# Kernel optimization log

Measured on AMD Instinct MI355X. Metric: run time of the kernel, lower is better.

## Reference

```python
import jax, jax.numpy as jnp
import numpy as np

B, N, DIM, H, DH = 2, 2048, 256, 4, 32


def setup_inputs() -> dict:
    key = jax.random.key(0)
    k0, k1, k2, k3, k4 = jax.random.split(key, 5)
    x = jax.random.normal(k0, (B, N, DIM), dtype=jnp.float32)
    pos_bias = jax.random.normal(k1, (H, N, N), dtype=jnp.float32) * 0.02
    focus_present_mask = jax.random.randint(k2, (B,), 0, 2).astype(bool)
    W_qkv = jax.random.normal(k3, (DIM, 3 * H * DH), dtype=jnp.float32) * 0.05
    W_out = jax.random.normal(k4, (H * DH, DIM), dtype=jnp.float32) * 0.05
    return {"x": x, "pos_bias": pos_bias, "focus_present_mask": focus_present_mask,
            "W_qkv": W_qkv, "W_out": W_out}


def reference(x, pos_bias, focus_present_mask, W_qkv, W_out):
    b, n, _ = x.shape
    scale = DH ** -0.5
    qkv = x @ W_qkv                                  # [b, n, 3*h*dh]
    q, k, v = jnp.split(qkv, 3, axis=-1)
    split_heads = lambda t: t.reshape(b, n, H, DH).transpose(0, 2, 1, 3)  # b h n d
    q, k, v = split_heads(q), split_heads(k), split_heads(v)
    q = q * scale
    sim = jnp.einsum('bhid,bhjd->bhij', q, k)        # [b, h, n, n]
    sim = sim + pos_bias[None]                       # additive relative-position bias
    # focus-present masking: batches with mask=True attend only to self (eye),
    # batches with mask=False attend everywhere -> always-apply form is equivalent.
    eye = jnp.eye(n, dtype=bool)
    mask = jnp.where(focus_present_mask[:, None, None, None], eye[None, None], True)
    neg = -jnp.finfo(sim.dtype).max
    sim = jnp.where(mask, sim, neg)
    sim = sim - jax.lax.stop_gradient(sim.max(axis=-1, keepdims=True))
    attn = jax.nn.softmax(sim, axis=-1)
    out = jnp.einsum('bhij,bhjd->bhid', attn, v)     # [b, h, n, d]
    out = out.transpose(0, 2, 1, 3).reshape(b, n, H * DH)
    return out @ W_out
```

## Files before the change

### kernel.cpp

```cpp
#include <hip/hip_runtime.h>
#include <hip/hip_bf16.h>

#define DEVI __device__ __forceinline__

typedef short bf16x8 __attribute__((ext_vector_type(8)));
typedef float f32x4 __attribute__((ext_vector_type(4)));
typedef unsigned short u16x4 __attribute__((ext_vector_type(4)));

static constexpr int B_ = 2, N_ = 2048, DIM_ = 256, H_ = 4, DH_ = 32;
static constexpr int NQKV_ = 3 * H_ * DH_;
static constexpr float SCALE_ = 0.17677669529663687f;

DEVI unsigned short f2bf(float f) {
  __hip_bfloat16 h = __float2bfloat16(f);
  return *reinterpret_cast<unsigned short*>(&h);
}

__global__ __launch_bounds__(256) void k_gemm_qkv(
    const float* __restrict__ X,
    const float* __restrict__ Wqkv,
    unsigned short* __restrict__ Qo,
    unsigned short* __restrict__ Ko,
    unsigned short* __restrict__ Vo,
    unsigned short* __restrict__ Vto) {
  constexpr int LDB = 258;
  __shared__ unsigned short Bts[64 * LDB];
  const int tid = threadIdx.x;
  const int col0b = blockIdx.y * 64;
  for (int p = tid; p < 64 * 256; p += 256) {
    const int col = p & 63;
    const int k = p >> 6;
    Bts[col * LDB + k] = f2bf(Wqkv[k * NQKV_ + col0b + col]);
  }
  __syncthreads();

  const int w = tid >> 6, l = tid & 63;
  const int lr = l & 15, g = l >> 4;
  const int row0 = blockIdx.x * 64 + (w >> 1) * 32;
  const int colw = (w & 1) * 32;
  const float* xr0 = X + (size_t)(row0 + lr) * 256;
  const float* xr1 = X + (size_t)(row0 + 16 + lr) * 256;
  f32x4 acc[2][2] = {};
#pragma unroll
  for (int kb = 0; kb < 256; kb += 32) {
    f32x4 xa = *(const f32x4*)(xr0 + kb + g * 8);
    f32x4 xb4 = *(const f32x4*)(xr0 + kb + g * 8 + 4);
    f32x4 xc = *(const f32x4*)(xr1 + kb + g * 8);
    f32x4 xd = *(const f32x4*)(xr1 + kb + g * 8 + 4);
    bf16x8 a0, a1;
#pragma unroll
    for (int j = 0; j < 4; j++) {
      a0[j] = (short)f2bf(xa[j]);
      a0[4 + j] = (short)f2bf(xb4[j]);
      a1[j] = (short)f2bf(xc[j]);
      a1[4 + j] = (short)f2bf(xd[j]);
    }
    bf16x8 b0 = *(const bf16x8*)(&Bts[(colw + lr) * LDB + kb + g * 8]);
    bf16x8 b1 = *(const bf16x8*)(&Bts[(colw + 16 + lr) * LDB + kb + g * 8]);
    acc[0][0] = __builtin_amdgcn_mfma_f32_16x16x32_bf16(a0, b0, acc[0][0], 0, 0, 0);
    acc[0][1] = __builtin_amdgcn_mfma_f32_16x16x32_bf16(a0, b1, acc[0][1], 0, 0, 0);
    acc[1][0] = __builtin_amdgcn_mfma_f32_16x16x32_bf16(a1, b0, acc[1][0], 0, 0, 0);
    acc[1][1] = __builtin_amdgcn_mfma_f32_16x16x32_bf16(a1, b1, acc[1][1], 0, 0, 0);
  }
#pragma unroll
  for (int mi = 0; mi < 2; mi++)
#pragma unroll
    for (int ni = 0; ni < 2; ni++) {
      const int colg = col0b + colw + ni * 16 + lr;
      const int sec = colg >> 7;
      const int h = (colg >> 5) & 3;
      const int d = colg & 31;
      const int rbase = row0 + mi * 16 + g * 4;
      const int bb = rbase >> 11;
      const int n0 = rbase & (N_ - 1);
      if (sec == 0) {
#pragma unroll
        for (int r = 0; r < 4; r++)
          Qo[((bb * H_ + h) * N_ + n0 + r) * DH_ + d] = f2bf(acc[mi][ni][r] * SCALE_);
      } else if (sec == 1) {
#pragma unroll
        for (int r = 0; r < 4; r++)
          Ko[((bb * H_ + h) * N_ + n0 + r) * DH_ + d] = f2bf(acc[mi][ni][r]);
      } else {
        u16x4 vp;
#pragma unroll
        for (int r = 0; r < 4; r++) {
          const unsigned short vb = f2bf(acc[mi][ni][r]);
          Vo[((bb * H_ + h) * N_ + n0 + r) * DH_ + d] = vb;
          vp[r] = vb;
        }
        const int c32 = n0 & ~31;
        const int local = n0 & 31;
        const int slot = ((local & 15) >> 2) * 8 + ((local >> 4) << 2);
        *(u16x4*)(Vto + ((bb * H_ + h) * DH_ + d) * N_ + c32 + slot) = vp;
      }
    }
}

__global__ __launch_bounds__(512) void k_attn_lds(
    const unsigned short* __restrict__ Q,
    const unsigned short* __restrict__ K,
    const unsigned short* __restrict__ Vt,
    const unsigned short* __restrict__ V,
    const float* __restrict__ bias,
    const int* __restrict__ mask,
    unsigned short* __restrict__ AO) {
  const int bh = blockIdx.y;
  const int b = bh >> 2, h = bh & 3;
  const int qt = blockIdx.x;
  const int tid = threadIdx.x;
  const int qb = qt * 16;
  if (mask[b] != 0) {
    if (tid < 64) {
      const int q = tid >> 2;
      const int d8 = (tid & 3) * 8;
      bf16x8 v = *(const bf16x8*)(V + ((size_t)bh * N_ + qb + q) * DH_ + d8);
      *(bf16x8*)(AO + (size_t)(b * N_ + qb + q) * (H_ * DH_) + h * DH_ + d8) = v;
    }
    return;
  }
  __shared__ float so[16][8][32];
  __shared__ float ss[16][8];
  const int w = tid >> 6, l = tid & 63, lr = l & 15, g = l >> 4;
  const int c0 = w * 256;
  const unsigned short* Kp = K + bh * N_ * DH_;
  const unsigned short* Vtp = Vt + bh * DH_ * N_;
  const float* biasrow = bias + (size_t)(h * N_ + qb + lr) * N_;
  const bf16x8 qf = *(const bf16x8*)(Q + (bh * N_ + qb + lr) * DH_ + g * 8);
  float s = 0.f;
  f32x4 o0 = {}, o1 = {};
  for (int c = c0; c < c0 + 256; c += 32) {
    bf16x8 k0 = *(const bf16x8*)(Kp + (c + lr) * DH_ + g * 8);
    bf16x8 k1 = *(const bf16x8*)(Kp + (c + 16 + lr) * DH_ + g * 8);
    f32x4 z = {};
    f32x4 st0 = __builtin_amdgcn_mfma_f32_16x16x32_bf16(k0, qf, z, 0, 0, 0);
    f32x4 st1 = __builtin_amdgcn_mfma_f32_16x16x32_bf16(k1, qf, z, 0, 0, 0);
    f32x4 bi0 = *(const f32x4*)(biasrow + c + g * 4);
    f32x4 bi1 = *(const f32x4*)(biasrow + c + 16 + g * 4);
    bf16x8 pf;
#pragma unroll
    for (int r = 0; r < 4; r++) {
      const float p0 = __expf(st0[r] + bi0[r]);
      const float p1 = __expf(st1[r] + bi1[r]);
      s += p0 + p1;
      pf[r] = (short)f2bf(p0);
      pf[4 + r] = (short)f2bf(p1);
    }
    bf16x8 v0 = *(const bf16x8*)(Vtp + lr * N_ + c + g * 8);
    bf16x8 v1 = *(const bf16x8*)(Vtp + (16 + lr) * N_ + c + g * 8);
    o0 = __builtin_amdgcn_mfma_f32_16x16x32_bf16(v0, pf, o0, 0, 0, 0);
    o1 = __builtin_amdgcn_mfma_f32_16x16x32_bf16(v1, pf, o1, 0, 0, 0);
  }
  s += __shfl_xor(s, 16);
  s += __shfl_xor(s, 32);
  *(f32x4*)&so[lr][w][g * 4] = o0;
  *(f32x4*)&so[lr][w][16 + g * 4] = o1;
  if (g == 0) ss[lr][w] = s;
  __syncthreads();
  {
    const int q = tid >> 5;
    const int d = tid & 31;
    float acc = 0.f, ssum = 0.f;
#pragma unroll
    for (int w2 = 0; w2 < 8; w2++) {
      acc += so[q][w2][d];
      ssum += ss[q][w2];
    }
    AO[(size_t)(b * N_ + qb + q) * (H_ * DH_) + h * DH_ + d] = f2bf(acc / ssum);
  }
}

__global__ __launch_bounds__(256) void k_gemm_out(
    const unsigned short* __restrict__ A,
    const float* __restrict__ Wout,
    float* __restrict__ out) {
  constexpr int LDB = 130;
  __shared__ unsigned short Bts[64 * LDB];
  const int tid = threadIdx.x;
  const int col0b = blockIdx.y * 64;
  for (int p = tid; p < 64 * 128; p += 256) {
    const int col = p & 63;
    const int k = p >> 6;
    Bts[col * LDB + k] = f2bf(Wout[k * 256 + col0b + col]);
  }
  __syncthreads();

  const int w = tid >> 6, l = tid & 63;
  const int lr = l & 15, g = l >> 4;
  const int row0 = blockIdx.x * 64 + (w >> 1) * 32;
  const int colw = (w & 1) * 32;
  f32x4 acc[2][2] = {};
#pragma unroll
  for (int kb = 0; kb < 128; kb += 32) {
    bf16x8 a0 = *(const bf16x8*)(A + (row0 + lr) * 128 + kb + g * 8);
    bf16x8 a1 = *(const bf16x8*)(A + (row0 + 16 + lr) * 128 + kb + g * 8);
    bf16x8 b0 = *(const bf16x8*)(&Bts[(colw + lr) * LDB + kb + g * 8]);
    bf16x8 b1 = *(const bf16x8*)(&Bts[(colw + 16 + lr) * LDB + kb + g * 8]);
    acc[0][0] = __builtin_amdgcn_mfma_f32_16x16x32_bf16(a0, b0, acc[0][0], 0, 0, 0);
    acc[0][1] = __builtin_amdgcn_mfma_f32_16x16x32_bf16(a0, b1, acc[0][1], 0, 0, 0);
    acc[1][0] = __builtin_amdgcn_mfma_f32_16x16x32_bf16(a1, b0, acc[1][0], 0, 0, 0);
    acc[1][1] = __builtin_amdgcn_mfma_f32_16x16x32_bf16(a1, b1, acc[1][1], 0, 0, 0);
  }
#pragma unroll
  for (int mi = 0; mi < 2; mi++)
#pragma unroll
    for (int ni = 0; ni < 2; ni++) {
      const int colg = col0b + colw + ni * 16 + lr;
      const int rbase = row0 + mi * 16 + g * 4;
#pragma unroll
      for (int r = 0; r < 4; r++)
        out[(size_t)(rbase + r) * 256 + colg] = acc[mi][ni][r];
    }
}

extern "C" void kernel_launch(void* const* d_in, const int* in_sizes, int n_in,
                              void* d_out, int out_size, void* d_ws, size_t ws_size,
                              hipStream_t stream) {
  const float* x = (const float*)d_in[0];
  const float* bias = (const float*)d_in[1];
  const int* mask = (const int*)d_in[2];
  const float* Wqkv = (const float*)d_in[3];
  const float* Wout = (const float*)d_in[4];
  float* out = (float*)d_out;
  char* ws = (char*)d_ws;

  unsigned short* Qb    = (unsigned short*)(ws + 0);
  unsigned short* Kb    = (unsigned short*)(ws + 1048576);
  unsigned short* Vb    = (unsigned short*)(ws + 2097152);
  unsigned short* Vtb   = (unsigned short*)(ws + 3145728);
  unsigned short* AOb   = (unsigned short*)(ws + 4194304);

  k_gemm_qkv<<<dim3(64, 6), dim3(256), 0, stream>>>(x, Wqkv, Qb, Kb, Vb, Vtb);
  k_attn_lds<<<dim3(128, B_ * H_), dim3(512), 0, stream>>>(
      Qb, Kb, Vtb, Vb, bias, mask, AOb);
  k_gemm_out<<<dim3(64, 4), dim3(256), 0, stream>>>(AOb, Wout, out);
}
```

Baseline: 45.04 us.

## Stage pos_bias tiles through double-buffered LDS with coalesced row loads

```diff
diff --git a/kernel.cpp b/kernel.cpp
--- a/kernel.cpp
+++ b/kernel.cpp
@@ -119,37 +119,64 @@
     }
     return;
   }
+  constexpr int LDBS = 258;
   __shared__ float so[16][8][32];
   __shared__ float ss[16][8];
+  __shared__ float bs[2][16][LDBS];
   const int w = tid >> 6, l = tid & 63, lr = l & 15, g = l >> 4;
-  const int c0 = w * 256;
+  const int srow = tid >> 5;
+  const int sidx = tid & 31;
+  const float* brow_g = bias + (size_t)(h * N_ + qb + srow) * N_;
   const unsigned short* Kp = K + bh * N_ * DH_;
   const unsigned short* Vtp = Vt + bh * DH_ * N_;
-  const float* biasrow = bias + (size_t)(h * N_ + qb + lr) * N_;
   const bf16x8 qf = *(const bf16x8*)(Q + (bh * N_ + qb + lr) * DH_ + g * 8);
+  {
+    f32x4 p0 = *(const f32x4*)(brow_g + sidx * 4);
+    f32x4 p1 = *(const f32x4*)(brow_g + 128 + sidx * 4);
+    *(f32x4*)&bs[0][srow][sidx * 4] = p0;
+    *(f32x4*)&bs[0][srow][128 + sidx * 4] = p1;
+  }
+  __syncthreads();
   float s = 0.f;
   f32x4 o0 = {}, o1 = {};
-  for (int c = c0; c < c0 + 256; c += 32) {
-    bf16x8 k0 = *(const bf16x8*)(Kp + (c + lr) * DH_ + g * 8);
-    bf16x8 k1 = *(const bf16x8*)(Kp + (c + 16 + lr) * DH_ + g * 8);
-    f32x4 z = {};
-    f32x4 st0 = __builtin_amdgcn_mfma_f32_16x16x32_bf16(k0, qf, z, 0, 0, 0);
-    f32x4 st1 = __builtin_amdgcn_mfma_f32_16x16x32_bf16(k1, qf, z, 0, 0, 0);
-    f32x4 bi0 = *(const f32x4*)(biasrow + c + g * 4);
-    f32x4 bi1 = *(const f32x4*)(biasrow + c + 16 + g * 4);
-    bf16x8 pf;
-#pragma unroll
-    for (int r = 0; r < 4; r++) {
-      const float p0 = __expf(st0[r] + bi0[r]);
-      const float p1 = __expf(st1[r] + bi1[r]);
-      s += p0 + p1;
-      pf[r] = (short)f2bf(p0);
-      pf[4 + r] = (short)f2bf(p1);
-    }
-    bf16x8 v0 = *(const bf16x8*)(Vtp + lr * N_ + c + g * 8);
-    bf16x8 v1 = *(const bf16x8*)(Vtp + (16 + lr) * N_ + c + g * 8);
-    o0 = __builtin_amdgcn_mfma_f32_16x16x32_bf16(v0, pf, o0, 0, 0, 0);
-    o1 = __builtin_amdgcn_mfma_f32_16x16x32_bf16(v1, pf, o1, 0, 0, 0);
+  int cur = 0;
+#pragma unroll
+  for (int ci = 0; ci < 8; ci++) {
+    f32x4 n0 = {}, n1 = {};
+    if (ci < 7) {
+      n0 = *(const f32x4*)(brow_g + (ci + 1) * 256 + sidx * 4);
+      n1 = *(const f32x4*)(brow_g + (ci + 1) * 256 + 128 + sidx * 4);
+    }
+    {
+      const int c = ci * 256 + w * 32;
+      bf16x8 k0 = *(const bf16x8*)(Kp + (c + lr) * DH_ + g * 8);
+      bf16x8 k1 = *(const bf16x8*)(Kp + (c + 16 + lr) * DH_ + g * 8);
+      f32x4 z = {};
+      f32x4 st0 = __builtin_amdgcn_mfma_f32_16x16x32_bf16(k0, qf, z, 0, 0, 0);
+      f32x4 st1 = __builtin_amdgcn_mfma_f32_16x16x32_bf16(k1, qf, z, 0, 0, 0);
+      f32x4 bi0 = *(const f32x4*)(&bs[cur][lr][w * 32 + g * 4]);
+      f32x4 bi1 = *(const f32x4*)(&bs[cur][lr][w * 32 + 16 + g * 4]);
+      bf16x8 pf;
+#pragma unroll
+      for (int r = 0; r < 4; r++) {
+        const float p0 = __expf(st0[r] + bi0[r]);
+        const float p1 = __expf(st1[r] + bi1[r]);
+        s += p0 + p1;
+        pf[r] = (short)f2bf(p0);
+        pf[4 + r] = (short)f2bf(p1);
+      }
+      bf16x8 v0 = *(const bf16x8*)(Vtp + lr * N_ + c + g * 8);
+      bf16x8 v1 = *(const bf16x8*)(Vtp + (16 + lr) * N_ + c + g * 8);
+      o0 = __builtin_amdgcn_mfma_f32_16x16x32_bf16(v0, pf, o0, 0, 0, 0);
+      o1 = __builtin_amdgcn_mfma_f32_16x16x32_bf16(v1, pf, o1, 0, 0, 0);
+    }
+    __syncthreads();
+    if (ci < 7) {
+      *(f32x4*)&bs[cur ^ 1][srow][sidx * 4] = n0;
+      *(f32x4*)&bs[cur ^ 1][srow][128 + sidx * 4] = n1;
+    }
+    __syncthreads();
+    cur ^= 1;
   }
   s += __shfl_xor(s, 16);
   s += __shfl_xor(s, 32);
```

After: 41.61 us. -7.6%, faster.

## Split attention keys across two blocks and merge partials in output GEMM

Applied to the files above, without the earlier changes.

```diff
diff --git a/kernel.cpp b/kernel.cpp
--- a/kernel.cpp
+++ b/kernel.cpp
@@ -14,6 +14,11 @@
 DEVI unsigned short f2bf(float f) {
   __hip_bfloat16 h = __float2bfloat16(f);
   return *reinterpret_cast<unsigned short*>(&h);
+}
+DEVI float bf2f(unsigned short u) {
+  union { unsigned int i; float f; } x;
+  x.i = ((unsigned int)u) << 16;
+  return x.f;
 }
 
 __global__ __launch_bounds__(256) void k_gemm_qkv(
@@ -97,60 +102,91 @@
     }
 }
 
-__global__ __launch_bounds__(512) void k_attn_lds(
+__global__ __launch_bounds__(512, 6) void k_attn_split2(
     const unsigned short* __restrict__ Q,
     const unsigned short* __restrict__ K,
     const unsigned short* __restrict__ Vt,
-    const unsigned short* __restrict__ V,
     const float* __restrict__ bias,
     const int* __restrict__ mask,
-    unsigned short* __restrict__ AO) {
-  const int bh = blockIdx.y;
+    float* __restrict__ PO,
+    float* __restrict__ PS) {
+  const int bh = blockIdx.z;
   const int b = bh >> 2, h = bh & 3;
-  const int qt = blockIdx.x;
+  if (mask[b] != 0) return;
+  const int qt = blockIdx.x, sp = blockIdx.y;
   const int tid = threadIdx.x;
   const int qb = qt * 16;
-  if (mask[b] != 0) {
-    if (tid < 64) {
-      const int q = tid >> 2;
-      const int d8 = (tid & 3) * 8;
-      bf16x8 v = *(const bf16x8*)(V + ((size_t)bh * N_ + qb + q) * DH_ + d8);
-      *(bf16x8*)(AO + (size_t)(b * N_ + qb + q) * (H_ * DH_) + h * DH_ + d8) = v;
-    }
-    return;
-  }
+  const int spbase = sp * 1024;
   __shared__ float so[16][8][32];
   __shared__ float ss[16][8];
+  __shared__ unsigned short bs[3][16][258];
   const int w = tid >> 6, l = tid & 63, lr = l & 15, g = l >> 4;
-  const int c0 = w * 256;
+  const int srow = tid >> 5;
+  const int sidx = tid & 31;
+  const float* brow = bias + (size_t)(h * N_ + qb + srow) * N_ + spbase;
   const unsigned short* Kp = K + bh * N_ * DH_;
   const unsigned short* Vtp = Vt + bh * DH_ * N_;
-  const float* biasrow = bias + (size_t)(h * N_ + qb + lr) * N_;
   const bf16x8 qf = *(const bf16x8*)(Q + (bh * N_ + qb + lr) * DH_ + g * 8);
   float s = 0.f;
   f32x4 o0 = {}, o1 = {};
-  for (int c = c0; c < c0 + 256; c += 32) {
-    bf16x8 k0 = *(const bf16x8*)(Kp + (c + lr) * DH_ + g * 8);
-    bf16x8 k1 = *(const bf16x8*)(Kp + (c + 16 + lr) * DH_ + g * 8);
-    f32x4 z = {};
-    f32x4 st0 = __builtin_amdgcn_mfma_f32_16x16x32_bf16(k0, qf, z, 0, 0, 0);
-    f32x4 st1 = __builtin_amdgcn_mfma_f32_16x16x32_bf16(k1, qf, z, 0, 0, 0);
-    f32x4 bi0 = *(const f32x4*)(biasrow + c + g * 4);
-    f32x4 bi1 = *(const f32x4*)(biasrow + c + 16 + g * 4);
-    bf16x8 pf;
-#pragma unroll
-    for (int r = 0; r < 4; r++) {
-      const float p0 = __expf(st0[r] + bi0[r]);
-      const float p1 = __expf(st1[r] + bi1[r]);
-      s += p0 + p1;
-      pf[r] = (short)f2bf(p0);
-      pf[4 + r] = (short)f2bf(p1);
-    }
-    bf16x8 v0 = *(const bf16x8*)(Vtp + lr * N_ + c + g * 8);
-    bf16x8 v1 = *(const bf16x8*)(Vtp + (16 + lr) * N_ + c + g * 8);
-    o0 = __builtin_amdgcn_mfma_f32_16x16x32_bf16(v0, pf, o0, 0, 0, 0);
-    o1 = __builtin_amdgcn_mfma_f32_16x16x32_bf16(v1, pf, o1, 0, 0, 0);
-  }
+
+#define BLOAD(PA, PB, CI)                                        \
+  {                                                              \
+    PA = *(const f32x4*)(brow + (CI) * 256 + sidx * 4);          \
+    PB = *(const f32x4*)(brow + (CI) * 256 + 128 + sidx * 4);    \
+  }
+#define BSTORE(BUF, PA, PB)                                      \
+  {                                                              \
+    u16x4 ua, ub;                                                \
+    _Pragma("unroll") for (int r = 0; r < 4; r++) {              \
+      ua[r] = f2bf(PA[r]);                                       \
+      ub[r] = f2bf(PB[r]);                                       \
+    }                                                            \
+    *(u16x4*)&bs[BUF][srow][sidx * 4] = ua;                      \
+    *(u16x4*)&bs[BUF][srow][128 + sidx * 4] = ub;                \
+  }
+#define ABODY(CI)                                                             \
+  {                                                                           \
+    const int c = spbase + (CI) * 256 + w * 32;                               \
+    bf16x8 k0 = *(const bf16x8*)(Kp + (c + lr) * DH_ + g * 8);                \
+    bf16x8 k1 = *(const bf16x8*)(Kp + (c + 16 + lr) * DH_ + g * 8);           \
+    f32x4 z = {};                                                             \
+    f32x4 st0 = __builtin_amdgcn_mfma_f32_16x16x32_bf16(k0, qf, z, 0, 0, 0);  \
+    f32x4 st1 = __builtin_amdgcn_mfma_f32_16x16x32_bf16(k1, qf, z, 0, 0, 0);  \
+    u16x4 ua = *(const u16x4*)&bs[(CI) % 3][lr][w * 32 + g * 4];              \
+    u16x4 ub = *(const u16x4*)&bs[(CI) % 3][lr][w * 32 + 16 + g * 4];         \
+    bf16x8 pf;                                                                \
+    _Pragma("unroll") for (int r = 0; r < 4; r++) {                           \
+      const float p0 = __expf(st0[r] + bf2f(ua[r]));                          \
+      const float p1 = __expf(st1[r] + bf2f(ub[r]));                          \
+      s += p0 + p1;                                                           \
+      pf[r] = (short)f2bf(p0);                                                \
+      pf[4 + r] = (short)f2bf(p1);                                            \
+    }                                                                         \
+    bf16x8 v0 = *(const bf16x8*)(Vtp + lr * N_ + c + g * 8);                  \
+    bf16x8 v1 = *(const bf16x8*)(Vtp + (16 + lr) * N_ + c + g * 8);           \
+    o0 = __builtin_amdgcn_mfma_f32_16x16x32_bf16(v0, pf, o0, 0, 0, 0);        \
+    o1 = __builtin_amdgcn_mfma_f32_16x16x32_bf16(v1, pf, o1, 0, 0, 0);        \
+  }
+
+  f32x4 pA0, pA1, pB0, pB1;
+  BLOAD(pA0, pA1, 0)
+  BLOAD(pB0, pB1, 1)
+  BSTORE(0, pA0, pA1)
+  __syncthreads();
+  BSTORE(1, pB0, pB1)
+  BLOAD(pA0, pA1, 2)
+  ABODY(0)
+  __syncthreads();
+  BSTORE(2, pA0, pA1)
+  BLOAD(pB0, pB1, 3)
+  ABODY(1)
+  __syncthreads();
+  BSTORE(0, pB0, pB1)
+  ABODY(2)
+  __syncthreads();
+  ABODY(3)
+
   s += __shfl_xor(s, 16);
   s += __shfl_xor(s, 32);
   *(f32x4*)&so[lr][w][g * 4] = o0;
@@ -166,12 +202,17 @@
       acc += so[q][w2][d];
       ssum += ss[q][w2];
     }
-    AO[(size_t)(b * N_ + qb + q) * (H_ * DH_) + h * DH_ + d] = f2bf(acc / ssum);
-  }
+    PO[((size_t)(bh * 2 + sp) * N_ + qb + q) * 32 + d] = acc;
+    if (d == 0) PS[(size_t)(bh * 2 + sp) * N_ + qb + q] = ssum;
+  }
+#undef BLOAD
+#undef BSTORE
+#undef ABODY
 }
 
 __global__ __launch_bounds__(256) void k_gemm_out(
-    const unsigned short* __restrict__ A,
+    const float* __restrict__ PO, const float* __restrict__ PS,
+    const unsigned short* __restrict__ V, const int* __restrict__ mask,
     const float* __restrict__ Wout,
     float* __restrict__ out) {
   constexpr int LDB = 130;
@@ -189,11 +230,41 @@
   const int lr = l & 15, g = l >> 4;
   const int row0 = blockIdx.x * 64 + (w >> 1) * 32;
   const int colw = (w & 1) * 32;
+  const int b = (blockIdx.x * 64) >> 11;
+  const bool msk = (mask[b] != 0);
+  const int na = (row0 + lr) & (N_ - 1);
+  const int nb2 = (row0 + 16 + lr) & (N_ - 1);
   f32x4 acc[2][2] = {};
 #pragma unroll
   for (int kb = 0; kb < 128; kb += 32) {
-    bf16x8 a0 = *(const bf16x8*)(A + (row0 + lr) * 128 + kb + g * 8);
-    bf16x8 a1 = *(const bf16x8*)(A + (row0 + 16 + lr) * 128 + kb + g * 8);
+    const int h = kb >> 5;
+    const int d0 = g * 8;
+    const int bh = b * H_ + h;
+    bf16x8 a0, a1;
+    if (msk) {
+      a0 = *(const bf16x8*)(V + ((size_t)bh * N_ + na) * DH_ + d0);
+      a1 = *(const bf16x8*)(V + ((size_t)bh * N_ + nb2) * DH_ + d0);
+    } else {
+      const size_t base0 = (size_t)(bh * 2 + 0) * N_;
+      const size_t base1 = (size_t)(bh * 2 + 1) * N_;
+      f32x4 xa0 = *(const f32x4*)(PO + (base0 + na) * 32 + d0);
+      f32x4 xa0h = *(const f32x4*)(PO + (base0 + na) * 32 + d0 + 4);
+      f32x4 xa1 = *(const f32x4*)(PO + (base1 + na) * 32 + d0);
+      f32x4 xa1h = *(const f32x4*)(PO + (base1 + na) * 32 + d0 + 4);
+      const float ia = 1.f / (PS[base0 + na] + PS[base1 + na]);
+      f32x4 xb0 = *(const f32x4*)(PO + (base0 + nb2) * 32 + d0);
+      f32x4 xb0h = *(const f32x4*)(PO + (base0 + nb2) * 32 + d0 + 4);
+      f32x4 xb1 = *(const f32x4*)(PO + (base1 + nb2) * 32 + d0);
+      f32x4 xb1h = *(const f32x4*)(PO + (base1 + nb2) * 32 + d0 + 4);
+      const float ib = 1.f / (PS[base0 + nb2] + PS[base1 + nb2]);
+#pragma unroll
+      for (int j = 0; j < 4; j++) {
+        a0[j] = (short)f2bf((xa0[j] + xa1[j]) * ia);
+        a0[4 + j] = (short)f2bf((xa0h[j] + xa1h[j]) * ia);
+        a1[j] = (short)f2bf((xb0[j] + xb1[j]) * ib);
+        a1[4 + j] = (short)f2bf((xb0h[j] + xb1h[j]) * ib);
+      }
+    }
     bf16x8 b0 = *(const bf16x8*)(&Bts[(colw + lr) * LDB + kb + g * 8]);
     bf16x8 b1 = *(const bf16x8*)(&Bts[(colw + 16 + lr) * LDB + kb + g * 8]);
     acc[0][0] = __builtin_amdgcn_mfma_f32_16x16x32_bf16(a0, b0, acc[0][0], 0, 0, 0);
@@ -224,14 +295,15 @@
   float* out = (float*)d_out;
   char* ws = (char*)d_ws;
 
-  unsigned short* Qb    = (unsigned short*)(ws + 0);
-  unsigned short* Kb    = (unsigned short*)(ws + 1048576);
-  unsigned short* Vb    = (unsigned short*)(ws + 2097152);
-  unsigned short* Vtb   = (unsigned short*)(ws + 3145728);
-  unsigned short* AOb   = (unsigned short*)(ws + 4194304);
+  unsigned short* Qb  = (unsigned short*)(ws + 0);
+  unsigned short* Kb  = (unsigned short*)(ws + 1048576);
+  unsigned short* Vb  = (unsigned short*)(ws + 2097152);
+  unsigned short* Vtb = (unsigned short*)(ws + 3145728);
+  float* PO           = (float*)(ws + 4194304);
+  float* PS           = (float*)(ws + 8388608);
 
   k_gemm_qkv<<<dim3(64, 6), dim3(256), 0, stream>>>(x, Wqkv, Qb, Kb, Vb, Vtb);
-  k_attn_lds<<<dim3(128, B_ * H_), dim3(512), 0, stream>>>(
-      Qb, Kb, Vtb, Vb, bias, mask, AOb);
-  k_gemm_out<<<dim3(64, 4), dim3(256), 0, stream>>>(AOb, Wout, out);
-}
+  k_attn_split2<<<dim3(128, 2, B_ * H_), dim3(512), 0, stream>>>(
+      Qb, Kb, Vtb, bias, mask, PO, PS);
+  k_gemm_out<<<dim3(64, 4), dim3(256), 0, stream>>>(PO, PS, Vb, mask, Wout, out);
+}
```

After: 49.65 us. +10.2%, slower.

## Split attention key range across two blocks and add combine kernel

Applied to the files above, without the earlier changes.

```diff
diff --git a/kernel.cpp b/kernel.cpp
--- a/kernel.cpp
+++ b/kernel.cpp
@@ -97,39 +97,33 @@
     }
 }
 
-__global__ __launch_bounds__(512) void k_attn_lds(
+__global__ __launch_bounds__(512, 6) void k_attn2(
     const unsigned short* __restrict__ Q,
     const unsigned short* __restrict__ K,
     const unsigned short* __restrict__ Vt,
-    const unsigned short* __restrict__ V,
     const float* __restrict__ bias,
     const int* __restrict__ mask,
-    unsigned short* __restrict__ AO) {
-  const int bh = blockIdx.y;
+    float* __restrict__ PO,
+    float* __restrict__ PS) {
+  const int bh = blockIdx.z;
   const int b = bh >> 2, h = bh & 3;
-  const int qt = blockIdx.x;
+  if (mask[b] != 0) return;
+  const int qt = blockIdx.x, sp = blockIdx.y;
   const int tid = threadIdx.x;
   const int qb = qt * 16;
-  if (mask[b] != 0) {
-    if (tid < 64) {
-      const int q = tid >> 2;
-      const int d8 = (tid & 3) * 8;
-      bf16x8 v = *(const bf16x8*)(V + ((size_t)bh * N_ + qb + q) * DH_ + d8);
-      *(bf16x8*)(AO + (size_t)(b * N_ + qb + q) * (H_ * DH_) + h * DH_ + d8) = v;
-    }
-    return;
-  }
   __shared__ float so[16][8][32];
   __shared__ float ss[16][8];
   const int w = tid >> 6, l = tid & 63, lr = l & 15, g = l >> 4;
-  const int c0 = w * 256;
+  const int c0 = sp * 1024 + w * 128;
   const unsigned short* Kp = K + bh * N_ * DH_;
   const unsigned short* Vtp = Vt + bh * DH_ * N_;
   const float* biasrow = bias + (size_t)(h * N_ + qb + lr) * N_;
   const bf16x8 qf = *(const bf16x8*)(Q + (bh * N_ + qb + lr) * DH_ + g * 8);
   float s = 0.f;
   f32x4 o0 = {}, o1 = {};
-  for (int c = c0; c < c0 + 256; c += 32) {
+#pragma unroll
+  for (int i = 0; i < 4; i++) {
+    const int c = c0 + i * 32;
     bf16x8 k0 = *(const bf16x8*)(Kp + (c + lr) * DH_ + g * 8);
     bf16x8 k1 = *(const bf16x8*)(Kp + (c + 16 + lr) * DH_ + g * 8);
     f32x4 z = {};
@@ -166,8 +160,42 @@
       acc += so[q][w2][d];
       ssum += ss[q][w2];
     }
-    AO[(size_t)(b * N_ + qb + q) * (H_ * DH_) + h * DH_ + d] = f2bf(acc / ssum);
-  }
+    PO[((size_t)(bh * 2 + sp) * N_ + qb + q) * 32 + d] = acc;
+    if (d == 0) PS[(size_t)(bh * 2 + sp) * N_ + qb + q] = ssum;
+  }
+}
+
+__global__ __launch_bounds__(256) void k_combine(
+    const float* __restrict__ PO, const float* __restrict__ PS,
+    const unsigned short* __restrict__ V, const int* __restrict__ mask,
+    unsigned short* __restrict__ AO) {
+  const int t = blockIdx.x * 256 + threadIdx.x;
+  const int d8 = (t & 3) * 8;
+  const int q = (t >> 2) & (N_ - 1);
+  const int h = (t >> 13) & (H_ - 1);
+  const int b = t >> 15;
+  const int bh = b * H_ + h;
+  unsigned short* dst = AO + ((size_t)(b * N_ + q)) * (H_ * DH_) + h * DH_ + d8;
+  if (mask[b] != 0) {
+    bf16x8 v = *(const bf16x8*)(V + ((size_t)bh * N_ + q) * DH_ + d8);
+    *(bf16x8*)dst = v;
+    return;
+  }
+  const size_t base0 = (size_t)(bh * 2 + 0) * N_ + q;
+  const size_t base1 = (size_t)(bh * 2 + 1) * N_ + q;
+  f32x4 a0 = *(const f32x4*)(PO + base0 * 32 + d8);
+  f32x4 a0h = *(const f32x4*)(PO + base0 * 32 + d8 + 4);
+  f32x4 a1 = *(const f32x4*)(PO + base1 * 32 + d8);
+  f32x4 a1h = *(const f32x4*)(PO + base1 * 32 + d8 + 4);
+  const float inv = 1.f / (PS[base0] + PS[base1]);
+  u16x4 w0, w1;
+#pragma unroll
+  for (int r = 0; r < 4; r++) {
+    w0[r] = f2bf((a0[r] + a1[r]) * inv);
+    w1[r] = f2bf((a0h[r] + a1h[r]) * inv);
+  }
+  *(u16x4*)dst = w0;
+  *(u16x4*)(dst + 4) = w1;
 }
 
 __global__ __launch_bounds__(256) void k_gemm_out(
@@ -224,14 +252,17 @@
   float* out = (float*)d_out;
   char* ws = (char*)d_ws;
 
-  unsigned short* Qb    = (unsigned short*)(ws + 0);
-  unsigned short* Kb    = (unsigned short*)(ws + 1048576);
-  unsigned short* Vb    = (unsigned short*)(ws + 2097152);
-  unsigned short* Vtb   = (unsigned short*)(ws + 3145728);
-  unsigned short* AOb   = (unsigned short*)(ws + 4194304);
+  unsigned short* Qb  = (unsigned short*)(ws + 0);
+  unsigned short* Kb  = (unsigned short*)(ws + 1048576);
+  unsigned short* Vb  = (unsigned short*)(ws + 2097152);
+  unsigned short* Vtb = (unsigned short*)(ws + 3145728);
+  unsigned short* AOb = (unsigned short*)(ws + 4194304);
+  float* PO           = (float*)(ws + 5242880);
+  float* PS           = (float*)(ws + 9437184);
 
   k_gemm_qkv<<<dim3(64, 6), dim3(256), 0, stream>>>(x, Wqkv, Qb, Kb, Vb, Vtb);
-  k_attn_lds<<<dim3(128, B_ * H_), dim3(512), 0, stream>>>(
-      Qb, Kb, Vtb, Vb, bias, mask, AOb);
+  k_attn2<<<dim3(128, 2, B_ * H_), dim3(512), 0, stream>>>(
+      Qb, Kb, Vtb, bias, mask, PO, PS);
+  k_combine<<<dim3(256), dim3(256), 0, stream>>>(PO, PS, Vb, mask, AOb);
   k_gemm_out<<<dim3(64, 4), dim3(256), 0, stream>>>(AOb, Wout, out);
 }
```

Measured after the change: 49.66 us. 1.1x slower.
